# Optimization experiments

Hardware: AMD Instinct MI355X
Metric: run time of the kernel (lower is better)

Reference implementation:

```python
import jax, jax.numpy as jnp
import numpy as np

N_NODES = 50000


def gcn_conv(x, edge_index, edge_weight, W, b):
    """PyG GCNConv: x' = D^{-1/2}(A+I)D^{-1/2} (x W) + b, with edge weights."""
    n = x.shape[0]
    x = x @ W  # transform first (PyG order): [N, d_out]
    row, col = edge_index[0], edge_index[1]  # source -> target
    # add self loops with weight 1
    loop = jnp.arange(n)
    row = jnp.concatenate([row, loop])
    col = jnp.concatenate([col, loop])
    ew = jnp.concatenate([edge_weight, jnp.ones((n,), dtype=x.dtype)])
    # symmetric normalization based on (weighted) in-degree at targets
    deg = jax.ops.segment_sum(ew, col, num_segments=n)
    dis = jnp.where(deg > 0, jax.lax.rsqrt(deg), 0.0)
    norm = dis[row] * ew * dis[col]  # [E+N]
    # gather-scale-scatter aggregation
    msg = x[row] * norm[:, None]  # [E+N, d_out]
    out = jax.ops.segment_sum(msg, col, num_segments=n)
    return out + b


def setup_inputs() -> dict:
    key = jax.random.key(0)
    ks = jax.random.split(key, 9)
    E = 800000
    bert_output = jax.random.normal(ks[0], (N_NODES, 1024), dtype=jnp.float32)
    edge_index = jax.random.randint(ks[1], (2, E), 0, N_NODES, dtype=jnp.int64)
    edge_weight = jax.random.uniform(ks[2], (E,), dtype=jnp.float32)
    s1 = 1.0 / np.sqrt(1024)
    s2 = 1.0 / np.sqrt(512)
    s3 = 1.0 / np.sqrt(128)
    W1 = jax.random.uniform(ks[3], (1024, 512), jnp.float32, -s1, s1)
    b1 = jnp.zeros((512,), jnp.float32)
    W2 = jax.random.uniform(ks[4], (512, 128), jnp.float32, -s2, s2)
    b2 = jnp.zeros((128,), jnp.float32)
    Wfc = jax.random.uniform(ks[5], (128, 14), jnp.float32, -s3, s3)
    bfc = jax.random.uniform(ks[6], (14,), jnp.float32, -s3, s3)
    return {
        "bert_output": bert_output,
        "edge_index": edge_index,
        "edge_weight": edge_weight,
        "W1": W1, "b1": b1, "W2": W2, "b2": b2, "Wfc": Wfc, "bfc": bfc,
    }


def reference(bert_output, edge_index, edge_weight, W1, b1, W2, b2, Wfc, bfc):
    h = jax.nn.relu(gcn_conv(bert_output, edge_index, edge_weight, W1, b1))
    h = jax.nn.relu(gcn_conv(h, edge_index, edge_weight, W2, b2))
    logits = h @ Wfc + bfc
    return jax.nn.sigmoid(logits)
```

## Files before the change

### kernel.cpp

```cpp
#include <hip/hip_runtime.h>
#include <stdint.h>

__device__ __forceinline__ float bf2f(unsigned short h) {
  union { uint32_t u; float f; } v; v.u = ((uint32_t)h) << 16; return v.f;
}
__device__ __forceinline__ unsigned short f2bf(float f) {
  union { float f; uint32_t u; } v; v.f = f;
  uint32_t u = v.u;
  u += 0x7FFFu + ((u >> 16) & 1u);
  return (unsigned short)(u >> 16);
}
__device__ __forceinline__ uint32_t pack2bf(float a, float b) {
  return (uint32_t)f2bf(a) | ((uint32_t)f2bf(b) << 16);
}
__device__ __forceinline__ int ld_idx(const void* p, size_t i, int is64) {
  return is64 ? (int)((const long long*)p)[i] : ((const int*)p)[i];
}
__device__ __forceinline__ float ld_w(const void* p, size_t i, int f32) {
  return f32 ? ((const float*)p)[i] : bf2f(((const unsigned short*)p)[i]);
}

typedef __attribute__((ext_vector_type(8))) short short8;
typedef __attribute__((ext_vector_type(4))) float floatx4;

__device__ __forceinline__ void gl2lds16(const unsigned short* g, unsigned short* l) {
  __builtin_amdgcn_global_load_lds(
      (const __attribute__((address_space(1))) uint32_t*)(const void*)g,
      (__attribute__((address_space(3))) uint32_t*)(void*)l,
      16, 0, 0);
}

__global__ void bgcn_probe(const uint32_t* __restrict__ xw,
                           const uint32_t* __restrict__ iw,
                           int* __restrict__ flags) {
  if (threadIdx.x == 0 && blockIdx.x == 0) {
    int hits = 0;
    for (int i = 0; i < 256; ++i) {
      uint32_t b = (xw[i] >> 8) & 0x7F;
      if (b >= 0x38 && b <= 0x41) hits++;
    }
    flags[0] = (hits < 128) ? 1 : 0;
    int nz = 0;
    for (int i = 1; i < 128; i += 2) nz += (iw[i] != 0);
    flags[1] = (nz == 0) ? 1 : 0;
  }
}

__global__ void bgcn_cvt8(const void* __restrict__ src, unsigned short* __restrict__ dst,
                          int n8, const int* __restrict__ flags) {
  int i = blockIdx.x * 256 + threadIdx.x;
  if (i >= n8) return;
  size_t o = (size_t)i * 8;
  uint4 d;
  if (flags[0]) {
    const float4* f = (const float4*)((const float*)src + o);
    float4 f0 = f[0], f1 = f[1];
    d = make_uint4(pack2bf(f0.x, f0.y), pack2bf(f0.z, f0.w),
                   pack2bf(f1.x, f1.y), pack2bf(f1.z, f1.w));
  } else {
    d = *(const uint4*)((const unsigned short*)src + o);
  }
  *(uint4*)(dst + o) = d;
}
__global__ __launch_bounds__(256) void bgcn_cvt_t(
    const void* __restrict__ src, unsigned short* __restrict__ dst,
    int K, int N, const int* __restrict__ flags) {
  __shared__ unsigned short tile[32][33];
  int k0 = blockIdx.x * 32, n0 = blockIdx.y * 32;
  int tx = threadIdx.x & 31, ty = threadIdx.x >> 5;
  bool f32 = flags[0];
  #pragma unroll
  for (int i = 0; i < 4; ++i) {
    size_t s = (size_t)(k0 + ty + i * 8) * N + n0 + tx;
    tile[ty + i * 8][tx] = f32 ? f2bf(((const float*)src)[s])
                               : ((const unsigned short*)src)[s];
  }
  __syncthreads();
  #pragma unroll
  for (int i = 0; i < 4; ++i)
    dst[(size_t)(n0 + ty + i * 8) * K + k0 + tx] = tile[tx][ty + i * 8];
}
__global__ void bgcn_cvt_small(const void* b1, const void* b2,
                               const void* wfc, const void* bfc,
                               unsigned short* db1, unsigned short* db2,
                               unsigned short* dwfc, unsigned short* dbfc,
                               const int* __restrict__ flags) {
  int i = blockIdx.x * 256 + threadIdx.x;
  bool f32 = flags[0];
  const void* s; unsigned short* d; int j;
  if (i < 512)            { s = b1;  d = db1;  j = i; }
  else if (i < 640)       { s = b2;  d = db2;  j = i - 512; }
  else if (i < 2432)      { s = wfc; d = dwfc; j = i - 640; }
  else if (i < 2446)      { s = bfc; d = dbfc; j = i - 2432; }
  else return;
  d[j] = f32 ? f2bf(((const float*)s)[j]) : ((const unsigned short*)s)[j];
}

__global__ void bgcn_init(float* __restrict__ deg, int* __restrict__ counts,
                          int* __restrict__ fill, int n) {
  int i = blockIdx.x * 256 + threadIdx.x;
  if (i < n) { deg[i] = 1.0f; counts[i] = 0; fill[i] = 0; }
}
__global__ void bgcn_deg_hist(const void* __restrict__ ei, const void* __restrict__ ew,
                              const int* __restrict__ flags,
                              float* __restrict__ deg, int* __restrict__ counts, int E) {
  int e = blockIdx.x * 256 + threadIdx.x;
  if (e >= E) return;
  int c = ld_idx(ei, (size_t)E + e, flags[1]);
  atomicAdd(&deg[c], ld_w(ew, e, flags[0]));
  atomicAdd(&counts[c], 1);
}
__global__ void bgcn_dis(const float* __restrict__ deg, float* __restrict__ dis, int n) {
  int i = blockIdx.x * 256 + threadIdx.x;
  if (i < n) dis[i] = rsqrtf(deg[i]);
}
__global__ void bgcn_scan_block(const int* __restrict__ counts, int* __restrict__ rowptr,
                                int* __restrict__ blocksum, int n) {
  __shared__ int buf[1024];
  int gid = blockIdx.x * 1024 + threadIdx.x;
  int v = (gid < n) ? counts[gid] : 0;
  buf[threadIdx.x] = v;
  __syncthreads();
  for (int off = 1; off < 1024; off <<= 1) {
    int x = (threadIdx.x >= off) ? buf[threadIdx.x - off] : 0;
    __syncthreads();
    buf[threadIdx.x] += x;
    __syncthreads();
  }
  if (gid < n) rowptr[gid + 1] = buf[threadIdx.x];
  if (threadIdx.x == 1023) blocksum[blockIdx.x] = buf[1023];
}
__global__ void bgcn_scan_tops(int* __restrict__ blocksum, int nb) {
  if (threadIdx.x == 0 && blockIdx.x == 0) {
    int acc = 0;
    for (int i = 0; i < nb; ++i) { int v = blocksum[i]; blocksum[i] = acc; acc += v; }
  }
}
__global__ void bgcn_scan_add(int* __restrict__ rowptr, const int* __restrict__ blocksum, int n) {
  int gid = blockIdx.x * 1024 + threadIdx.x;
  if (gid < n) rowptr[gid + 1] += blocksum[blockIdx.x];
  if (gid == 0) rowptr[0] = 0;
}
__global__ void bgcn_scatter(const void* __restrict__ ei, const void* __restrict__ ew,
                             const int* __restrict__ flags,
                             const float* __restrict__ dis,
                             const int* __restrict__ rowptr, int* __restrict__ fill,
                             int* __restrict__ esrc, float* __restrict__ enorm, int E) {
  int e = blockIdx.x * 256 + threadIdx.x;
  if (e >= E) return;
  int is64 = flags[1];
  int r = ld_idx(ei, e, is64), c = ld_idx(ei, (size_t)E + e, is64);
  int pos = rowptr[c] + atomicAdd(&fill[c], 1);
  esrc[pos]  = r;
  enorm[pos] = dis[r] * ld_w(ew, e, flags[0]) * dis[c];
}

__global__ __launch_bounds__(256) void bgcn_gemm_lds(
    const unsigned short* __restrict__ A,
    const unsigned short* __restrict__ Bt,
    unsigned short* __restrict__ C,
    int M, int N, int K, int nblk_bits) {
  __shared__ unsigned short Abuf[128 * 32];
  __shared__ unsigned short Bbuf[128 * 32];
  int t = threadIdx.x;
  int wave = t >> 6, lane = t & 63;
  int bx = blockIdx.x;
  int nblk = bx & ((1 << nblk_bits) - 1);
  int mblk = bx >> nblk_bits;
  int m0 = mblk * 128, n0 = nblk * 128;

  floatx4 acc[4][4];
  #pragma unroll
  for (int i = 0; i < 4; ++i)
    #pragma unroll
    for (int j = 0; j < 4; ++j)
      #pragma unroll
      for (int r = 0; r < 4; ++r) acc[i][j][r] = 0.0f;

  int rii  = lane >> 2;
  int koff = (lane & 3) * 8;
  int ar0 = m0 + wave * 32 + rii;      if (ar0 >= M) ar0 = M - 1;
  int ar1 = m0 + wave * 32 + 16 + rii; if (ar1 >= M) ar1 = M - 1;
  const unsigned short* Ag0 = A + (size_t)ar0 * K + koff;
  const unsigned short* Ag1 = A + (size_t)ar1 * K + koff;
  const unsigned short* Bg0 = Bt + (size_t)(n0 + wave * 32 + rii) * K + koff;
  const unsigned short* Bg1 = Bg0 + (size_t)16 * K;
  unsigned short* Al0 = Abuf + (wave * 32) * 32 + lane * 8;
  unsigned short* Al1 = Abuf + (wave * 32 + 16) * 32 + lane * 8;
  unsigned short* Bl0 = Bbuf + (wave * 32) * 32 + lane * 8;
  unsigned short* Bl1 = Bbuf + (wave * 32 + 16) * 32 + lane * 8;

  int fr = lane & 15;
  int fk = (lane >> 4) * 8;
  int mw = (wave & 1) * 64;
  int nw = (wave >> 1) * 64;

  for (int k0 = 0; k0 < K; k0 += 32) {
    gl2lds16(Ag0 + k0, Al0);
    gl2lds16(Ag1 + k0, Al1);
    gl2lds16(Bg0 + k0, Bl0);
    gl2lds16(Bg1 + k0, Bl1);
    __syncthreads();

    short8 afr[4], bfr[4];
    #pragma unroll
    for (int i = 0; i < 4; ++i)
      afr[i] = *(const short8*)(Abuf + (mw + i * 16 + fr) * 32 + fk);
    #pragma unroll
    for (int i = 0; i < 4; ++i)
      bfr[i] = *(const short8*)(Bbuf + (nw + i * 16 + fr) * 32 + fk);
    #pragma unroll
    for (int mt = 0; mt < 4; ++mt)
      #pragma unroll
      for (int nt = 0; nt < 4; ++nt)
        acc[mt][nt] = __builtin_amdgcn_mfma_f32_16x16x32_bf16(afr[mt], bfr[nt], acc[mt][nt], 0, 0, 0);
    __syncthreads();
  }

  int col_l = lane & 15;
  int row_b = (lane >> 4) * 4;
  #pragma unroll
  for (int mt = 0; mt < 4; ++mt)
    #pragma unroll
    for (int nt = 0; nt < 4; ++nt)
      #pragma unroll
      for (int r = 0; r < 4; ++r) {
        int m = m0 + mw + mt * 16 + row_b + r;
        if (m < M)
          C[(size_t)m * N + n0 + nw + nt * 16 + col_l] = f2bf(acc[mt][nt][r]);
      }
}

#define GST 40
__global__ __launch_bounds__(256, 2) void bgcn_gemm128(
    const void* __restrict__ Araw, int a_probe, const int* __restrict__ flags,
    const unsigned short* __restrict__ Bt,
    unsigned short* __restrict__ C,
    int M, int N, int K, int nblk_bits) {
  __shared__ unsigned short Abuf[128 * GST];
  __shared__ unsigned short Bbuf[128 * GST];
  const bool a_fp32 = a_probe && flags[0];
  int t = threadIdx.x;
  int wave = t >> 6, lane = t & 63;
  int bx = blockIdx.x;
  int nblk = bx & ((1 << nblk_bits) - 1);
  int mblk = bx >> nblk_bits;
  int m0 = mblk * 128, n0 = nblk * 128;

  floatx4 acc[4][4];
  #pragma unroll
  for (int i = 0; i < 4; ++i)
    #pragma unroll
    for (int j = 0; j < 4; ++j)
      #pragma unroll
      for (int r = 0; r < 4; ++r) acc[i][j][r] = 0.0f;

  int srow  = t >> 1;
  int skoff = (t & 1) * 16;
  int am = m0 + srow; if (am >= M) am = M - 1;
  const float*          Af = (const float*)Araw          + (size_t)am * K + skoff;
  const unsigned short* Ah = (const unsigned short*)Araw + (size_t)am * K + skoff;
  const unsigned short* Bp = Bt + (size_t)(n0 + srow) * K + skoff;
  unsigned short* AL = Abuf + srow * GST + skoff;
  unsigned short* BL = Bbuf + srow * GST + skoff;

  int fr = lane & 15;
  int fk = (lane >> 4) * 8;
  int mw = (wave & 1) * 64;
  int nw = (wave >> 1) * 64;

  for (int k0 = 0; k0 < K; k0 += 32) {
    uint4 a0, a1;
    if (a_fp32) {
      float4 f0 = *(const float4*)(Af + k0);
      float4 f1 = *(const float4*)(Af + k0 + 4);
      float4 f2 = *(const float4*)(Af + k0 + 8);
      float4 f3 = *(const float4*)(Af + k0 + 12);
      a0 = make_uint4(pack2bf(f0.x, f0.y), pack2bf(f0.z, f0.w),
                      pack2bf(f1.x, f1.y), pack2bf(f1.z, f1.w));
      a1 = make_uint4(pack2bf(f2.x, f2.y), pack2bf(f2.z, f2.w),
                      pack2bf(f3.x, f3.y), pack2bf(f3.z, f3.w));
    } else {
      a0 = *(const uint4*)(Ah + k0);
      a1 = *(const uint4*)(Ah + k0 + 8);
    }
    uint4 b0 = *(const uint4*)(Bp + k0);
    uint4 b1 = *(const uint4*)(Bp + k0 + 8);
    *(uint4*)AL       = a0;
    *(uint4*)(AL + 8) = a1;
    *(uint4*)BL       = b0;
    *(uint4*)(BL + 8) = b1;
    __syncthreads();

    short8 afr[4], bfr[4];
    #pragma unroll
    for (int i = 0; i < 4; ++i)
      afr[i] = *(const short8*)(Abuf + (mw + i * 16 + fr) * GST + fk);
    #pragma unroll
    for (int i = 0; i < 4; ++i)
      bfr[i] = *(const short8*)(Bbuf + (nw + i * 16 + fr) * GST + fk);
    #pragma unroll
    for (int mt = 0; mt < 4; ++mt)
      #pragma unroll
      for (int nt = 0; nt < 4; ++nt)
        acc[mt][nt] = __builtin_amdgcn_mfma_f32_16x16x32_bf16(afr[mt], bfr[nt], acc[mt][nt], 0, 0, 0);
    __syncthreads();
  }

  int col_l = lane & 15;
  int row_b = (lane >> 4) * 4;
  #pragma unroll
  for (int mt = 0; mt < 4; ++mt)
    #pragma unroll
    for (int nt = 0; nt < 4; ++nt)
      #pragma unroll
      for (int r = 0; r < 4; ++r) {
        int m = m0 + mw + mt * 16 + row_b + r;
        if (m < M)
          C[(size_t)m * N + n0 + nw + nt * 16 + col_l] = f2bf(acc[mt][nt][r]);
      }
}

__device__ __forceinline__ void accum8(float* acc, uint4 r, float w) {
  acc[0] += w * bf2f((unsigned short)(r.x & 0xffff));
  acc[1] += w * bf2f((unsigned short)(r.x >> 16));
  acc[2] += w * bf2f((unsigned short)(r.y & 0xffff));
  acc[3] += w * bf2f((unsigned short)(r.y >> 16));
  acc[4] += w * bf2f((unsigned short)(r.z & 0xffff));
  acc[5] += w * bf2f((unsigned short)(r.z >> 16));
  acc[6] += w * bf2f((unsigned short)(r.w & 0xffff));
  acc[7] += w * bf2f((unsigned short)(r.w >> 16));
}
__device__ __forceinline__ void accum2(float* acc, uint32_t r, float w) {
  acc[0] += w * bf2f((unsigned short)(r & 0xffff));
  acc[1] += w * bf2f((unsigned short)(r >> 16));
}

template <int F>
__global__ __launch_bounds__(256) void bgcn_aggregate(
    const unsigned short* __restrict__ H,
    const int* __restrict__ rowptr,
    const int* __restrict__ esrc,
    const float* __restrict__ enorm,
    const float* __restrict__ dis,
    const unsigned short* __restrict__ bias,
    unsigned short* __restrict__ Out,
    int n_nodes) {
  constexpr int VPL = F / 64;
  int lane = threadIdx.x & 63;
  int c = blockIdx.x * 4 + (threadIdx.x >> 6);
  if (c >= n_nodes) return;
  float acc[VPL];
  #pragma unroll
  for (int j = 0; j < VPL; ++j) acc[j] = 0.0f;

  int beg = rowptr[c], end = rowptr[c + 1];
  const unsigned short* Hl = H + (size_t)lane * VPL;

  if (end > beg) {
    for (int e = beg; e < end; e += 8) {
      int   s[8]; float w[8];
      #pragma unroll
      for (int q = 0; q < 8; ++q) {
        int idx = e + q;
        int ii  = idx < end ? idx : end - 1;
        s[q] = esrc[ii];
        w[q] = idx < end ? enorm[ii] : 0.0f;
      }
      if constexpr (VPL == 8) {
        uint4 r[8];
        #pragma unroll
        for (int q = 0; q < 8; ++q) r[q] = *(const uint4*)(Hl + (size_t)s[q] * F);
        #pragma unroll
        for (int q = 0; q < 8; ++q) accum8(acc, r[q], w[q]);
      } else {
        uint32_t r[8];
        #pragma unroll
        for (int q = 0; q < 8; ++q) r[q] = *(const uint32_t*)(Hl + (size_t)s[q] * F);
        #pragma unroll
        for (int q = 0; q < 8; ++q) accum2(acc, r[q], w[q]);
      }
    }
  }

  float ds = dis[c];
  float wself = ds * ds;
  if constexpr (VPL == 8) {
    uint4 rs = *(const uint4*)(Hl + (size_t)c * F);
    accum8(acc, rs, wself);
  } else {
    uint32_t rs = *(const uint32_t*)(Hl + (size_t)c * F);
    accum2(acc, rs, wself);
  }

  unsigned short ob[VPL];
  #pragma unroll
  for (int j = 0; j < VPL; ++j) {
    float v = acc[j] + bf2f(bias[lane * VPL + j]);
    ob[j] = f2bf(fmaxf(v, 0.0f));
  }
  if constexpr (VPL == 8) {
    uint4 st = make_uint4((uint32_t)ob[0] | ((uint32_t)ob[1] << 16),
                          (uint32_t)ob[2] | ((uint32_t)ob[3] << 16),
                          (uint32_t)ob[4] | ((uint32_t)ob[5] << 16),
                          (uint32_t)ob[6] | ((uint32_t)ob[7] << 16));
    *(uint4*)(Out + (size_t)c * F + lane * VPL) = st;
  } else {
    *(uint32_t*)(Out + (size_t)c * F + lane * VPL) =
        (uint32_t)ob[0] | ((uint32_t)ob[1] << 16);
  }
}

__global__ __launch_bounds__(256) void bgcn_fc_sigmoid(
    const unsigned short* __restrict__ X,
    const unsigned short* __restrict__ W,
    const unsigned short* __restrict__ b,
    float* __restrict__ out,
    int n_nodes) {
  __shared__ float Ws[128 * 14];
  __shared__ float bs[14];
  for (int i = threadIdx.x; i < 128 * 14; i += 256) Ws[i] = bf2f(W[i]);
  if (threadIdx.x < 14) bs[threadIdx.x] = bf2f(b[threadIdx.x]);
  __syncthreads();
  int node = blockIdx.x * 256 + threadIdx.x;
  if (node >= n_nodes) return;
  float acc[14];
  #pragma unroll
  for (int c = 0; c < 14; ++c) acc[c] = bs[c];
  const unsigned short* xp = X + (size_t)node * 128;
  for (int k8 = 0; k8 < 16; ++k8) {
    uint4 r = *(const uint4*)(xp + k8 * 8);
    float xv[8];
    xv[0] = bf2f((unsigned short)(r.x & 0xffff)); xv[1] = bf2f((unsigned short)(r.x >> 16));
    xv[2] = bf2f((unsigned short)(r.y & 0xffff)); xv[3] = bf2f((unsigned short)(r.y >> 16));
    xv[4] = bf2f((unsigned short)(r.z & 0xffff)); xv[5] = bf2f((unsigned short)(r.z >> 16));
    xv[6] = bf2f((unsigned short)(r.w & 0xffff)); xv[7] = bf2f((unsigned short)(r.w >> 16));
    #pragma unroll
    for (int j = 0; j < 8; ++j) {
      int k = k8 * 8 + j;
      #pragma unroll
      for (int c = 0; c < 14; ++c) acc[c] = fmaf(xv[j], Ws[k * 14 + c], acc[c]);
    }
  }
  float* op = out + (size_t)node * 14;
  #pragma unroll
  for (int c = 0; c < 14; ++c)
    op[c] = 1.0f / (1.0f + __expf(-acc[c]));
}

static inline size_t padsz(size_t x) { return (x + 255) & ~(size_t)255; }
static inline void* wsa(char*& p, size_t bytes) {
  void* r = p;
  p += padsz(bytes);
  return r;
}

extern "C" void kernel_launch(void* const* d_in, const int* in_sizes, int n_in,
                              void* d_out, int out_size, void* d_ws, size_t ws_size,
                              hipStream_t stream) {
  const void* Xr   = d_in[0];
  const void* EIr  = d_in[1];
  const void* EWr  = d_in[2];
  const void* W1r  = d_in[3];
  const void* b1r  = d_in[4];
  const void* W2r  = d_in[5];
  const void* b2r  = d_in[6];
  const void* Wfcr = d_in[7];
  const void* bfcr = d_in[8];
  float* out = (float*)d_out;

  const int N = in_sizes[0] / 1024;
  const int E = in_sizes[2];

  size_t need = padsz((size_t)N * 512 * 2)
              + padsz((size_t)N * 1024 * 2)
              + 4 * padsz((size_t)N * 4)
              + padsz((size_t)(N + 1) * 4)
              + padsz(256 * 4)
              + 2 * padsz((size_t)E * 4)
              + padsz(1024 * 512 * 2) + padsz(512 * 128 * 2)
              + padsz(512 * 2) + padsz(128 * 2) + padsz(128 * 14 * 2)
              + padsz(32) + padsz(8);
  const bool big = ws_size >= need;

  char* p = (char*)d_ws;
  unsigned short* R1  = (unsigned short*)wsa(p, (size_t)N * 512 * 2);
  unsigned short* R2  = (unsigned short*)wsa(p, (size_t)N * (big ? 1024 : 512) * 2);
  float* deg      = (float*)wsa(p, (size_t)N * 4);
  float* dis      = (float*)wsa(p, (size_t)N * 4);
  int*   counts   = (int*)wsa(p, (size_t)N * 4);
  int*   fill     = (int*)wsa(p, (size_t)N * 4);
  int*   rowptr   = (int*)wsa(p, (size_t)(N + 1) * 4);
  int*   blocksum = (int*)wsa(p, 256 * 4);
  int*   esrc     = (int*)wsa(p, (size_t)E * 4);
  float* enorm    = (float*)wsa(p, (size_t)E * 4);
  unsigned short* W1t  = (unsigned short*)wsa(p, (size_t)1024 * 512 * 2);
  unsigned short* W2t  = (unsigned short*)wsa(p, (size_t)512 * 128 * 2);
  unsigned short* b1c  = (unsigned short*)wsa(p, 512 * 2);
  unsigned short* b2c  = (unsigned short*)wsa(p, 128 * 2);
  unsigned short* Wfcc = (unsigned short*)wsa(p, 128 * 14 * 2);
  unsigned short* bfcc = (unsigned short*)wsa(p, 32);
  int* flags      = (int*)wsa(p, 8);

  unsigned short* H1  = R1;
  unsigned short* Xbf = R2;
  unsigned short* X2  = R2;
  unsigned short* H2  = R1;
  unsigned short* X3  = R1 + (size_t)N * 128;

  int gN = (N + 255) / 256;
  int gE = (E + 255) / 256;

  bgcn_probe<<<1, 64, 0, stream>>>((const uint32_t*)Xr, (const uint32_t*)EIr, flags);
  { dim3 g(1024 / 32, 512 / 32); bgcn_cvt_t<<<g, 256, 0, stream>>>(W1r, W1t, 1024, 512, flags); }
  { dim3 g(512 / 32, 128 / 32);  bgcn_cvt_t<<<g, 256, 0, stream>>>(W2r, W2t, 512, 128, flags); }
  bgcn_cvt_small<<<10, 256, 0, stream>>>(b1r, b2r, Wfcr, bfcr, b1c, b2c, Wfcc, bfcc, flags);
  if (big) {
    int n8 = N * 1024 / 8;
    bgcn_cvt8<<<(n8 + 255) / 256, 256, 0, stream>>>(Xr, Xbf, n8, flags);
  }

  bgcn_init<<<gN, 256, 0, stream>>>(deg, counts, fill, N);
  bgcn_deg_hist<<<gE, 256, 0, stream>>>(EIr, EWr, flags, deg, counts, E);
  bgcn_dis<<<gN, 256, 0, stream>>>(deg, dis, N);
  int nb = (N + 1023) / 1024;
  bgcn_scan_block<<<nb, 1024, 0, stream>>>(counts, rowptr, blocksum, N);
  bgcn_scan_tops<<<1, 64, 0, stream>>>(blocksum, nb);
  bgcn_scan_add<<<nb, 1024, 0, stream>>>(rowptr, blocksum, N);
  bgcn_scatter<<<gE, 256, 0, stream>>>(EIr, EWr, flags, dis, rowptr, fill, esrc, enorm, E);

  int mblks = (N + 127) / 128;

  if (big)
    bgcn_gemm_lds<<<mblks * 4, 256, 0, stream>>>(Xbf, W1t, H1, N, 512, 1024, 2);
  else
    bgcn_gemm128<<<mblks * 4, 256, 0, stream>>>(Xr, 1, flags, W1t, H1, N, 512, 1024, 2);
  bgcn_aggregate<512><<<(N + 3) / 4, 256, 0, stream>>>(H1, rowptr, esrc, enorm, dis, b1c, X2, N);

  bgcn_gemm_lds<<<mblks, 256, 0, stream>>>(X2, W2t, H2, N, 128, 512, 0);
  bgcn_aggregate<128><<<(N + 3) / 4, 256, 0, stream>>>(H2, rowptr, esrc, enorm, dis, b2c, X3, N);

  bgcn_fc_sigmoid<<<gN, 256, 0, stream>>>(X3, Wfcc, bfcc, out, N);
}
```

Before: 745.4 us.

## Split wide-feature aggregation across two wavefronts and batch edge loads via readlane

The SpMM aggregation kernel now assigns two wavefronts per node for the 512-wide layer, so each lane handles 4 features instead of 8. Edge indices and weights are loaded cooperatively, 64 per wave, and broadcast with readlane instead of every lane reading them redundantly. Gathers are issued 16 deep to keep more memory requests in flight. Self-row and bias loads are hoisted before the edge loop. The aim is more memory-level parallelism and less redundant index traffic, at the cost of reading each node's edge list twice for the 512 layer and higher register pressure.

```diff
diff --git a/kernel.cpp b/kernel.cpp
--- a/kernel.cpp
+++ b/kernel.cpp
@@ -321,22 +321,18 @@
       }
 }
 
-__device__ __forceinline__ void accum8(float* acc, uint4 r, float w) {
+__device__ __forceinline__ void accum4(float* acc, uint2 r, float w) {
   acc[0] += w * bf2f((unsigned short)(r.x & 0xffff));
   acc[1] += w * bf2f((unsigned short)(r.x >> 16));
   acc[2] += w * bf2f((unsigned short)(r.y & 0xffff));
   acc[3] += w * bf2f((unsigned short)(r.y >> 16));
-  acc[4] += w * bf2f((unsigned short)(r.z & 0xffff));
-  acc[5] += w * bf2f((unsigned short)(r.z >> 16));
-  acc[6] += w * bf2f((unsigned short)(r.w & 0xffff));
-  acc[7] += w * bf2f((unsigned short)(r.w >> 16));
 }
 __device__ __forceinline__ void accum2(float* acc, uint32_t r, float w) {
   acc[0] += w * bf2f((unsigned short)(r & 0xffff));
   acc[1] += w * bf2f((unsigned short)(r >> 16));
 }
 
-template <int F>
+template <int F, int WPN>
 __global__ __launch_bounds__(256) void bgcn_aggregate(
     const unsigned short* __restrict__ H,
     const int* __restrict__ rowptr,
@@ -346,67 +342,89 @@
     const unsigned short* __restrict__ bias,
     unsigned short* __restrict__ Out,
     int n_nodes) {
-  constexpr int VPL = F / 64;
-  int lane = threadIdx.x & 63;
-  int c = blockIdx.x * 4 + (threadIdx.x >> 6);
+  constexpr int FPW = F / WPN;
+  constexpr int VPL = FPW / 64;
+  constexpr int NPB = 4 / WPN;
+  constexpr int DEPTH = 16;
+
+  int t = threadIdx.x;
+  int lane = t & 63;
+  int wid = __builtin_amdgcn_readfirstlane(t >> 6);
+  int c = blockIdx.x * NPB + wid / WPN;
   if (c >= n_nodes) return;
+  c = __builtin_amdgcn_readfirstlane(c);
+  int h = wid % WPN;
+
+  int beg = __builtin_amdgcn_readfirstlane(rowptr[c]);
+  int end = __builtin_amdgcn_readfirstlane(rowptr[c + 1]);
+  float ds = dis[c];
+
+  int fo = h * FPW + lane * VPL;
+  const unsigned short* Hl = H + fo;
+
+  uint2 rs;
+  union { uint2 v; unsigned short u[4]; } bu;
+  if constexpr (VPL == 4) {
+    rs = *(const uint2*)(Hl + (size_t)c * F);
+    bu.v = *(const uint2*)(bias + fo);
+  } else {
+    rs.x = *(const uint32_t*)(Hl + (size_t)c * F);
+    bu.v.x = *(const uint32_t*)(bias + fo);
+  }
+
   float acc[VPL];
   #pragma unroll
   for (int j = 0; j < VPL; ++j) acc[j] = 0.0f;
 
-  int beg = rowptr[c], end = rowptr[c + 1];
-  const unsigned short* Hl = H + (size_t)lane * VPL;
-
-  if (end > beg) {
-    for (int e = beg; e < end; e += 8) {
-      int   s[8]; float w[8];
-      #pragma unroll
-      for (int q = 0; q < 8; ++q) {
-        int idx = e + q;
-        int ii  = idx < end ? idx : end - 1;
-        s[q] = esrc[ii];
-        w[q] = idx < end ? enorm[ii] : 0.0f;
+  for (int base = beg; base < end; base += 64) {
+    int n = end - base;
+    if (n > 64) n = 64;
+    n = __builtin_amdgcn_readfirstlane(n);
+    int   sv = 0;
+    float wv = 0.0f;
+    if (lane < n) {
+      sv = esrc[base + lane];
+      wv = enorm[base + lane];
+    }
+    for (int q0 = 0; q0 < n; q0 += DEPTH) {
+      uint2 r[DEPTH];
+      float w[DEPTH];
+      #pragma unroll
+      for (int j = 0; j < DEPTH; ++j) {
+        int q = q0 + j;
+        int qs = (q < n) ? q : 0;
+        int sq = __builtin_amdgcn_readlane(sv, qs);
+        w[j] = __int_as_float(
+            __builtin_amdgcn_readlane(__float_as_int(wv), q));
+        const unsigned short* src = Hl + (size_t)sq * F;
+        if constexpr (VPL == 4) r[j] = *(const uint2*)src;
+        else                    r[j].x = *(const uint32_t*)src;
       }
-      if constexpr (VPL == 8) {
-        uint4 r[8];
-        #pragma unroll
-        for (int q = 0; q < 8; ++q) r[q] = *(const uint4*)(Hl + (size_t)s[q] * F);
-        #pragma unroll
-        for (int q = 0; q < 8; ++q) accum8(acc, r[q], w[q]);
-      } else {
-        uint32_t r[8];
-        #pragma unroll
-        for (int q = 0; q < 8; ++q) r[q] = *(const uint32_t*)(Hl + (size_t)s[q] * F);
-        #pragma unroll
-        for (int q = 0; q < 8; ++q) accum2(acc, r[q], w[q]);
+      #pragma unroll
+      for (int j = 0; j < DEPTH; ++j) {
+        if constexpr (VPL == 4) accum4(acc, r[j], w[j]);
+        else                    accum2(acc, r[j].x, w[j]);
       }
     }
   }
 
-  float ds = dis[c];
   float wself = ds * ds;
-  if constexpr (VPL == 8) {
-    uint4 rs = *(const uint4*)(Hl + (size_t)c * F);
-    accum8(acc, rs, wself);
+  if constexpr (VPL == 4) accum4(acc, rs, wself);
+  else                    accum2(acc, rs.x, wself);
+
+  unsigned short ob[VPL];
+  #pragma unroll
+  for (int j = 0; j < VPL; ++j) {
+    float v = acc[j] + bf2f(bu.u[j]);
+    ob[j] = f2bf(fmaxf(v, 0.0f));
+  }
+  if constexpr (VPL == 4) {
+    uint2 st;
+    st.x = (uint32_t)ob[0] | ((uint32_t)ob[1] << 16);
+    st.y = (uint32_t)ob[2] | ((uint32_t)ob[3] << 16);
+    *(uint2*)(Out + (size_t)c * F + fo) = st;
   } else {
-    uint32_t rs = *(const uint32_t*)(Hl + (size_t)c * F);
-    accum2(acc, rs, wself);
-  }
-
-  unsigned short ob[VPL];
-  #pragma unroll
-  for (int j = 0; j < VPL; ++j) {
-    float v = acc[j] + bf2f(bias[lane * VPL + j]);
-    ob[j] = f2bf(fmaxf(v, 0.0f));
-  }
-  if constexpr (VPL == 8) {
-    uint4 st = make_uint4((uint32_t)ob[0] | ((uint32_t)ob[1] << 16),
-                          (uint32_t)ob[2] | ((uint32_t)ob[3] << 16),
-                          (uint32_t)ob[4] | ((uint32_t)ob[5] << 16),
-                          (uint32_t)ob[6] | ((uint32_t)ob[7] << 16));
-    *(uint4*)(Out + (size_t)c * F + lane * VPL) = st;
-  } else {
-    *(uint32_t*)(Out + (size_t)c * F + lane * VPL) =
+    *(uint32_t*)(Out + (size_t)c * F + fo) =
         (uint32_t)ob[0] | ((uint32_t)ob[1] << 16);
   }
 }
@@ -535,10 +553,10 @@
     bgcn_gemm_lds<<<mblks * 4, 256, 0, stream>>>(Xbf, W1t, H1, N, 512, 1024, 2);
   else
     bgcn_gemm128<<<mblks * 4, 256, 0, stream>>>(Xr, 1, flags, W1t, H1, N, 512, 1024, 2);
-  bgcn_aggregate<512><<<(N + 3) / 4, 256, 0, stream>>>(H1, rowptr, esrc, enorm, dis, b1c, X2, N);
+  bgcn_aggregate<512, 2><<<(N + 1) / 2, 256, 0, stream>>>(H1, rowptr, esrc, enorm, dis, b1c, X2, N);
 
   bgcn_gemm_lds<<<mblks, 256, 0, stream>>>(X2, W2t, H2, N, 128, 512, 0);
-  bgcn_aggregate<128><<<(N + 3) / 4, 256, 0, stream>>>(H2, rowptr, esrc, enorm, dis, b2c, X3, N);
+  bgcn_aggregate<128, 1><<<(N + 3) / 4, 256, 0, stream>>>(H2, rowptr, esrc, enorm, dis, b2c, X3, N);
 
   bgcn_fc_sigmoid<<<gN, 256, 0, stream>>>(X3, Wfcc, bfcc, out, N);
 }
```

Result: no change. 738.5 us (-0.9%).
